# Kernel tuning notes

Hardware: AMD Instinct MI355X
Metric: run time of the kernel (lower is better)

Reference implementation:

```python
import jax, jax.numpy as jnp
import numpy as np

N_HEADS = 16
EPS = 1e-6  # WanSelfAttention passes eps=1e-6 to WanRMSNorm
ROPE_MAX = 1024


def _rmsnorm(v, g):
    # WanRMSNorm: normalize in fp32 over the full `dim`, then scale by weight
    v32 = v.astype(jnp.float32)
    n = v32 * jax.lax.rsqrt(jnp.mean(v32 * v32, axis=-1, keepdims=True) + EPS)
    return n * g


def _rope(x, f, h, w, fc, fs):
    # x: [b, s, n, d] with s == f*h*w. Complex rope: (a+bi) * (cos + i sin)
    b, s, n, d = x.shape
    c = d // 2
    c1 = c - 2 * (c // 3)
    c2 = c // 3

    def build(t):  # t: [ROPE_MAX, c] -> [1, s, 1, c]
        tf, th, tw = t[:, :c1], t[:, c1:c1 + c2], t[:, c1 + c2:]
        pf = jnp.broadcast_to(tf[:f, None, None, :], (f, h, w, c1))
        ph = jnp.broadcast_to(th[None, :h, None, :], (f, h, w, c2))
        pw = jnp.broadcast_to(tw[None, None, :w, :], (f, h, w, c2))
        return jnp.concatenate([pf, ph, pw], axis=-1).reshape(1, f * h * w, 1, c)

    cosv, sinv = build(fc), build(fs)
    xr = x.astype(jnp.float32).reshape(b, s, n, c, 2)
    a, bi = xr[..., 0], xr[..., 1]
    out_r = a * cosv - bi * sinv
    out_i = a * sinv + bi * cosv
    return jnp.stack([out_r, out_i], axis=-1).reshape(b, s, n, d)


def setup_inputs() -> dict:
    key = jax.random.key(0)
    ks = jax.random.split(key, 12)
    b, s, dim = 1, 2048, 2048
    n, d = N_HEADS, 2048 // N_HEADS  # d = 128, c = 64
    f, h, w = 2, 32, 32              # f*h*w == s
    c = d // 2
    c1 = c - 2 * (c // 3)
    c2 = c // 3

    # Realistic rope tables per band (cos/sin of pos * inv_freq)
    pos = np.arange(ROPE_MAX, dtype=np.float64)[:, None]
    ang = []
    for cx in (c1, c2, c2):
        inv = 1.0 / (10000.0 ** (np.arange(cx, dtype=np.float64) / cx))
        ang.append(pos * inv[None, :])
    ang = np.concatenate(ang, axis=1)
    freqs_cos = jnp.asarray(np.cos(ang), dtype=jnp.float32)
    freqs_sin = jnp.asarray(np.sin(ang), dtype=jnp.float32)

    scale = 1.0 / np.sqrt(dim)
    inp = {
        "x": jax.random.normal(ks[0], (b, s, dim), dtype=jnp.float32),
        "freqs_cos": freqs_cos,
        "freqs_sin": freqs_sin,
        "Wq": jax.random.normal(ks[1], (dim, dim), dtype=jnp.float32) * scale,
        "bq": jnp.zeros((dim,), dtype=jnp.float32),
        "Wk": jax.random.normal(ks[2], (dim, dim), dtype=jnp.float32) * scale,
        "bk": jnp.zeros((dim,), dtype=jnp.float32),
        "Wv": jax.random.normal(ks[3], (dim, dim), dtype=jnp.float32) * scale,
        "bv": jnp.zeros((dim,), dtype=jnp.float32),
        "Wo": jax.random.normal(ks[4], (dim, dim), dtype=jnp.float32) * scale,
        "bo": jnp.zeros((dim,), dtype=jnp.float32),
        "gq": jnp.ones((dim,), dtype=jnp.float32),
        "gk": jnp.ones((dim,), dtype=jnp.float32),
        "seq_lens": jnp.array([s], dtype=jnp.int32),
        "f": f,
        "h": h,
        "w": w,
    }
    return inp


def reference(x, freqs_cos, freqs_sin, Wq, bq, Wk, bk, Wv, bv, Wo, bo, gq, gk,
              seq_lens, f, h, w):
    b, s, dim = x.shape
    n = N_HEADS
    d = dim // n

    q = _rmsnorm(x @ Wq.T + bq, gq).reshape(b, s, n, d)
    k = _rmsnorm(x @ Wk.T + bk, gk).reshape(b, s, n, d)
    v = (x @ Wv.T + bv).reshape(b, s, n, d)

    q = _rope(q, f, h, w, freqs_cos, freqs_sin)
    k = _rope(k, f, h, w, freqs_cos, freqs_sin)

    scale = np.float32(1.0 / np.sqrt(d))
    scores = jnp.einsum('bqnd,bknd->bnqk', q, k) * scale  # [b,n,s,s]
    key_mask = jnp.arange(s)[None, :] < seq_lens[:, None]  # [b,s] (k_lens)
    scores = jnp.where(key_mask[:, None, None, :], scores, -jnp.inf)
    probs = jax.nn.softmax(scores, axis=-1)
    out = jnp.einsum('bnqk,bknd->bqnd', probs, v).reshape(b, s, dim)
    return out @ Wo.T + bo
```

## Files before the change

### kernel.cpp

```cpp
#include <hip/hip_runtime.h>
#include <cstdint>
#include <cmath>

typedef unsigned int uint;
typedef unsigned short ushort;
typedef __bf16 bf16_t;
typedef bf16_t bf16x8 __attribute__((ext_vector_type(8)));
typedef float f32x4 __attribute__((ext_vector_type(4)));
typedef float f32x16 __attribute__((ext_vector_type(16)));

#define LOG2E 1.44269504088896340736f

__device__ __forceinline__ ushort f2bf(float f) {
  uint x = __float_as_uint(f);
  x += 0x7fffu + ((x >> 16) & 1u);
  return (ushort)(x >> 16);
}
__device__ __forceinline__ uint pack2(float lo, float hi) {
  return (uint)f2bf(lo) | ((uint)f2bf(hi) << 16);
}
__device__ __forceinline__ uint cvt_pk_bf16(float lo, float hi) {
  uint r;
  asm("v_cvt_pk_bf16_f32 %0, %1, %2" : "=v"(r) : "v"(lo), "v"(hi));
  return r;
}

__device__ __forceinline__ void gload_lds16(const void* gsrc, void* ldsdst) {
  typedef const __attribute__((address_space(1))) unsigned int* gp_t;
  typedef __attribute__((address_space(3))) unsigned int* lp_t;
  __builtin_amdgcn_global_load_lds((gp_t)(uintptr_t)gsrc,
                                   (lp_t)(unsigned int)(uintptr_t)ldsdst,
                                   16, 0, 0);
}

__global__ __launch_bounds__(256) void cvt5(const float* __restrict__ x,
                                            const float* __restrict__ wq,
                                            const float* __restrict__ wk,
                                            const float* __restrict__ wv,
                                            const float* __restrict__ wo,
                                            ushort* __restrict__ xb,
                                            ushort* __restrict__ wqkv,
                                            ushort* __restrict__ wob,
                                            int nx8, int nw8) {
  const int y = blockIdx.y;
  const float* src;
  ushort* dst;
  int n8;
  if (y == 0)      { src = x;  dst = xb;  n8 = nx8; }
  else if (y == 4) { src = wo; dst = wob; n8 = nw8; }
  else {
    src = (y == 1) ? wq : (y == 2) ? wk : wv;
    dst = wqkv + (size_t)(y - 1) * nw8 * 8;
    n8 = nw8;
  }
  int i = blockIdx.x * blockDim.x + threadIdx.x;
  if (i >= n8) return;
  const float4* s4 = (const float4*)src;
  float4 a = s4[i * 2], b = s4[i * 2 + 1];
  uint4 o;
  o.x = pack2(a.x, a.y); o.y = pack2(a.z, a.w);
  o.z = pack2(b.x, b.y); o.w = pack2(b.z, b.w);
  ((uint4*)dst)[i] = o;
}

__global__ __launch_bounds__(512) void gemm_qkv_db(const ushort* __restrict__ A,
                                                   const ushort* __restrict__ B,
                                                   const float* __restrict__ bq,
                                                   const float* __restrict__ bk,
                                                   const float* __restrict__ bv,
                                                   float* __restrict__ qpre,
                                                   float* __restrict__ kpre,
                                                   ushort* __restrict__ Vt,
                                                   int K, int S_) {
  __shared__ __align__(16) unsigned char As[16384];
  __shared__ __align__(16) unsigned char Bs[16384];
  const int t = threadIdx.x, l = t & 63, w = t >> 6;
  const int g = l >> 4, c = l & 15;
  const int wr = w >> 1, wc = w & 1;
  const int tm = blockIdx.y * 128, tn = blockIdx.x * 128;

  const int srow = w * 16 + (l >> 2);
  const int schunk = (l & 3) ^ (srow & 3);
  const ushort* Ag = A + (size_t)(tm + srow) * K + schunk * 8;
  const ushort* Bg = B + (size_t)(tn + srow) * K + schunk * 8;

  f32x4 acc[2][4] = {};

  const int NT = K >> 5;
  gload_lds16(Ag, As + w * 1024);
  gload_lds16(Bg, Bs + w * 1024);

  for (int j = 0; j < NT; ++j) {
    const int buf = j & 1, nb = buf ^ 1;
    if (j + 1 < NT) {
      const int kt1 = (j + 1) << 5;
      gload_lds16(Ag + kt1, As + nb * 8192 + w * 1024);
      gload_lds16(Bg + kt1, Bs + nb * 8192 + w * 1024);
      asm volatile("s_waitcnt vmcnt(2)" ::: "memory");
    } else {
      asm volatile("s_waitcnt vmcnt(0)" ::: "memory");
    }
    __builtin_amdgcn_s_barrier();

    const unsigned char* Ab = As + buf * 8192;
    const unsigned char* Bb = Bs + buf * 8192;
    bf16x8 af[2], bfr[4];
#pragma unroll
    for (int m = 0; m < 2; ++m) {
      int row = wr * 32 + m * 16 + c;
      af[m] = *(const bf16x8*)(Ab + row * 64 + ((g ^ (row & 3)) << 4));
    }
#pragma unroll
    for (int n = 0; n < 4; ++n) {
      int row = wc * 64 + n * 16 + c;
      bfr[n] = *(const bf16x8*)(Bb + row * 64 + ((g ^ (row & 3)) << 4));
    }
#pragma unroll
    for (int m = 0; m < 2; ++m)
#pragma unroll
      for (int n = 0; n < 4; ++n)
        acc[m][n] = __builtin_amdgcn_mfma_f32_16x16x32_bf16(af[m], bfr[n], acc[m][n], 0, 0, 0);

    __builtin_amdgcn_s_barrier();
  }

  const int sel = tn >> 11;
  if (sel < 2) {
    float* outp = sel ? kpre : qpre;
    const float* bias = sel ? bk : bq;
#pragma unroll
    for (int n = 0; n < 4; ++n) {
      int col = (tn & 2047) + wc * 64 + n * 16 + c;
      float bvv = bias[col];
#pragma unroll
      for (int m = 0; m < 2; ++m) {
        int row0 = tm + wr * 32 + m * 16 + g * 4;
#pragma unroll
        for (int i = 0; i < 4; ++i)
          outp[(size_t)(row0 + i) * 2048 + col] = acc[m][n][i] + bvv;
      }
    }
  } else {
#pragma unroll
    for (int n = 0; n < 4; ++n) {
      int colv = (tn - 4096) + wc * 64 + n * 16 + c;
      float bvv = bv[colv];
#pragma unroll
      for (int m = 0; m < 2; ++m) {
        int row0 = tm + wr * 32 + m * 16 + g * 4;
        uint2 o;
        o.x = pack2(acc[m][n][0] + bvv, acc[m][n][1] + bvv);
        o.y = pack2(acc[m][n][2] + bvv, acc[m][n][3] + bvv);
        *(uint2*)(Vt + (size_t)colv * S_ + row0) = o;
      }
    }
  }
}

__global__ __launch_bounds__(512) void gemm_wo_db(const ushort* __restrict__ A,
                                                  const ushort* __restrict__ B,
                                                  float* __restrict__ pbuf, int K) {
  __shared__ __align__(16) unsigned char As[16384];
  __shared__ __align__(16) unsigned char Bs[16384];
  const int t = threadIdx.x, l = t & 63, w = t >> 6;
  const int g = l >> 4, c = l & 15;
  const int wr = w >> 1, wc = w & 1;
  const int tm = blockIdx.y * 128, tn = blockIdx.x * 128;
  const int ks = blockIdx.z;
  const int k0 = ks * (K >> 1);

  const int srow = w * 16 + (l >> 2);
  const int schunk = (l & 3) ^ (srow & 3);
  const ushort* Ag = A + (size_t)(tm + srow) * K + k0 + schunk * 8;
  const ushort* Bg = B + (size_t)(tn + srow) * K + k0 + schunk * 8;

  f32x4 acc[2][4] = {};

  const int NT = K >> 6;
  gload_lds16(Ag, As + w * 1024);
  gload_lds16(Bg, Bs + w * 1024);

  for (int j = 0; j < NT; ++j) {
    const int buf = j & 1, nb = buf ^ 1;
    if (j + 1 < NT) {
      const int kt1 = (j + 1) << 5;
      gload_lds16(Ag + kt1, As + nb * 8192 + w * 1024);
      gload_lds16(Bg + kt1, Bs + nb * 8192 + w * 1024);
      asm volatile("s_waitcnt vmcnt(2)" ::: "memory");
    } else {
      asm volatile("s_waitcnt vmcnt(0)" ::: "memory");
    }
    __builtin_amdgcn_s_barrier();

    const unsigned char* Ab = As + buf * 8192;
    const unsigned char* Bb = Bs + buf * 8192;
    bf16x8 af[2], bfr[4];
#pragma unroll
    for (int m = 0; m < 2; ++m) {
      int row = wr * 32 + m * 16 + c;
      af[m] = *(const bf16x8*)(Ab + row * 64 + ((g ^ (row & 3)) << 4));
    }
#pragma unroll
    for (int n = 0; n < 4; ++n) {
      int row = wc * 64 + n * 16 + c;
      bfr[n] = *(const bf16x8*)(Bb + row * 64 + ((g ^ (row & 3)) << 4));
    }
#pragma unroll
    for (int m = 0; m < 2; ++m)
#pragma unroll
      for (int n = 0; n < 4; ++n)
        acc[m][n] = __builtin_amdgcn_mfma_f32_16x16x32_bf16(af[m], bfr[n], acc[m][n], 0, 0, 0);

    __builtin_amdgcn_s_barrier();
  }

  float* out = pbuf + (size_t)ks * 2048 * 2048;
#pragma unroll
  for (int n = 0; n < 4; ++n) {
    int col = tn + wc * 64 + n * 16 + c;
#pragma unroll
    for (int m = 0; m < 2; ++m) {
      int row0 = tm + wr * 32 + m * 16 + g * 4;
#pragma unroll
      for (int i = 0; i < 4; ++i)
        out[(size_t)(row0 + i) * 2048 + col] = acc[m][n][i];
    }
  }
}

__global__ __launch_bounds__(256) void reduce_wo(const float* __restrict__ p,
                                                 const float* __restrict__ bo,
                                                 float* __restrict__ out, int n4) {
  int i = blockIdx.x * blockDim.x + threadIdx.x;
  if (i >= n4) return;
  float4 a = ((const float4*)p)[i];
  float4 b = ((const float4*)p)[i + n4];
  float4 bb = *(const float4*)(bo + ((i * 4) & 2047));
  float4 o;
  o.x = a.x + b.x + bb.x; o.y = a.y + b.y + bb.y;
  o.z = a.z + b.z + bb.z; o.w = a.w + b.w + bb.w;
  ((float4*)out)[i] = o;
}

__global__ __launch_bounds__(256) void fuse_rms_rope(const float* __restrict__ qpre,
                                                     const float* __restrict__ kpre,
                                                     const float* __restrict__ gq,
                                                     const float* __restrict__ gk,
                                                     const float* __restrict__ fc,
                                                     const float* __restrict__ fs,
                                                     const int* __restrict__ pH,
                                                     const int* __restrict__ pW,
                                                     ushort* __restrict__ Qb,
                                                     ushort* __restrict__ Kb,
                                                     int dim, float foldq) {
  const int which = blockIdx.y;
  const float* pre = which ? kpre : qpre;
  const float* gw = which ? gk : gq;
  ushort* outp = which ? Kb : Qb;
  const float fold = which ? 1.0f : foldq;

  const int p = blockIdx.x, t = threadIdx.x;
  const float* row = pre + (size_t)p * dim;
  float v[8];
  {
    float4 a = *(const float4*)(row + t * 8);
    float4 b = *(const float4*)(row + t * 8 + 4);
    v[0] = a.x; v[1] = a.y; v[2] = a.z; v[3] = a.w;
    v[4] = b.x; v[5] = b.y; v[6] = b.z; v[7] = b.w;
  }
  float ss = 0.f;
#pragma unroll
  for (int i = 0; i < 8; ++i) ss += v[i] * v[i];
#pragma unroll
  for (int off = 32; off; off >>= 1) ss += __shfl_xor(ss, off);
  __shared__ float wsum[4];
  if ((t & 63) == 0) wsum[t >> 6] = ss;
  __syncthreads();
  float rstd = rsqrtf((wsum[0] + wsum[1] + wsum[2] + wsum[3]) * (1.0f / dim) + 1e-6f);
  float gv[8];
  {
    float4 a = *(const float4*)(gw + t * 8);
    float4 b = *(const float4*)(gw + t * 8 + 4);
    gv[0] = a.x; gv[1] = a.y; gv[2] = a.z; gv[3] = a.w;
    gv[4] = b.x; gv[5] = b.y; gv[6] = b.z; gv[7] = b.w;
  }
#pragma unroll
  for (int i = 0; i < 8; ++i) v[i] = v[i] * rstd * gv[i];

  const int H = pH[0], W = pW[0];
  const int hw = H * W;
  const int fr = p / hw;
  const int rem = p - fr * hw;
  const int hh = rem / W;
  const int ww = rem - hh * W;
  const int hd = dim / 16;
  const int cd = hd >> 1;
  const int c2 = cd / 3, c1 = cd - 2 * c2;
  const int j0 = ((t * 8) % hd) >> 1;

  uint ob[4];
#pragma unroll
  for (int q = 0; q < 4; ++q) {
    int j = j0 + q;
    int ri = (j < c1) ? fr : ((j < c1 + c2) ? hh : ww);
    float cs = fc[ri * cd + j];
    float sn = fs[ri * cd + j];
    float a = v[2 * q], b = v[2 * q + 1];
    ob[q] = pack2((a * cs - b * sn) * fold, (a * sn + b * cs) * fold);
  }
  uint4 o4; o4.x = ob[0]; o4.y = ob[1]; o4.z = ob[2]; o4.w = ob[3];
  *(uint4*)(outp + (size_t)p * dim + t * 8) = o4;
}

__global__ __launch_bounds__(512, 2) void attn32(const ushort* __restrict__ Qb,
                                                 const ushort* __restrict__ Kb,
                                                 const ushort* __restrict__ Vt,
                                                 ushort* __restrict__ Ob,
                                                 const int* __restrict__ seq_lens,
                                                 int S_, int DIMc) {
  __shared__ __align__(16) unsigned char smem[66560];
  float* mlbuf = (float*)(smem + 65536);
  const int t = threadIdx.x, l = t & 63, w = t >> 6;
  const int qsub = w & 3, ksp = w >> 2;
  const int h = l >> 5, ql = l & 31;

  const int orig = blockIdx.y * gridDim.x + blockIdx.x;
  const int nwg = gridDim.x * gridDim.y;
  const int lin = (orig & 7) * (nwg >> 3) + (orig >> 3);
  const int q0 = (lin % gridDim.x) * 128;
  const int head = lin / gridDim.x;
  const int kvlen = seq_lens[0];

  unsigned char* sk_s = smem + ksp * 16384;
  unsigned char* sv_s = smem + 32768 + ksp * 16384;

  bf16x8 qf[8];
  {
    const ushort* qp = Qb + (size_t)(q0 + qsub * 32 + ql) * DIMc + head * 128 + h * 8;
#pragma unroll
    for (int s = 0; s < 8; ++s) qf[s] = *(const bf16x8*)(qp + s * 16);
  }

  f32x16 ofr[4] = {};
  float m_run = -1e30f, l_run = 0.f;

  const int nt = (kvlen + 63) >> 6;
  const int half = (nt + 1) >> 1;
  const int tbase = ksp ? half : 0;
  const int mycnt = ksp ? (nt - half) : half;

  for (int tt = 0; tt < half; ++tt) {
    __syncthreads();
    if (tt < mycnt) {
      const int kv0 = (tbase + tt) * 64;
#pragma unroll
      for (int it = 0; it < 4; ++it) {
        int kr = qsub * 16 + it * 4 + (l >> 4);
        int kc = (l & 15) ^ (kr & 15);
        gload_lds16(Kb + (size_t)(kv0 + kr) * DIMc + head * 128 + kc * 8,
                    sk_s + qsub * 4096 + it * 1024);
        int vr = qsub * 32 + it * 8 + (l >> 3);
        int vc = (l & 7) ^ (vr & 7);
        gload_lds16(Vt + (size_t)(head * 128 + vr) * S_ + kv0 + vc * 8,
                    sv_s + qsub * 4096 + it * 1024);
      }
    }
    __syncthreads();
    if (tt >= mycnt) continue;
    const int kv0 = (tbase + tt) * 64;

    f32x16 sfr[2] = {};
    __builtin_amdgcn_s_setprio(1);
#pragma unroll
    for (int kb = 0; kb < 2; ++kb) {
      const unsigned char* kbp = sk_s + (kb * 32 + ql) * 256;
      const int rx = (kb * 32 + ql) & 15;
#pragma unroll
      for (int s = 0; s < 8; ++s) {
        bf16x8 kf = *(const bf16x8*)(kbp + (((s * 2 + h) ^ rx) << 4));
        sfr[kb] = __builtin_amdgcn_mfma_f32_32x32x16_bf16(kf, qf[s], sfr[kb], 0, 0, 0);
      }
    }
    __builtin_amdgcn_s_setprio(0);

    if (kv0 + 64 > kvlen) {
#pragma unroll
      for (int kb = 0; kb < 2; ++kb)
#pragma unroll
        for (int r = 0; r < 16; ++r) {
          int key = kv0 + kb * 32 + (r & 3) + 8 * (r >> 2) + 4 * h;
          if (key >= kvlen) sfr[kb][r] = -1e30f;
        }
    }

    float mt = -1e30f;
#pragma unroll
    for (int kb = 0; kb < 2; ++kb)
#pragma unroll
      for (int r = 0; r < 16; ++r) mt = fmaxf(mt, sfr[kb][r]);
    mt = fmaxf(mt, __shfl_xor(mt, 32));

    if (!__all(mt <= m_run + 8.0f)) {
      float m_new = fmaxf(m_run, mt);
      float fac = __builtin_amdgcn_exp2f(m_run - m_new);
      l_run *= fac;
#pragma unroll
      for (int df = 0; df < 4; ++df) ofr[df] *= fac;
      m_run = m_new;
    }

    float ls = 0.f;
    uint u[2][4][2];
#pragma unroll
    for (int kb = 0; kb < 2; ++kb)
#pragma unroll
      for (int G = 0; G < 4; ++G) {
        float p0 = __builtin_amdgcn_exp2f(sfr[kb][G * 4 + 0] - m_run);
        float p1 = __builtin_amdgcn_exp2f(sfr[kb][G * 4 + 1] - m_run);
        float p2 = __builtin_amdgcn_exp2f(sfr[kb][G * 4 + 2] - m_run);
        float p3 = __builtin_amdgcn_exp2f(sfr[kb][G * 4 + 3] - m_run);
        ls += (p0 + p1) + (p2 + p3);
        u[kb][G][0] = cvt_pk_bf16(p0, p1);
        u[kb][G][1] = cvt_pk_bf16(p2, p3);
      }
    ls += __shfl_xor(ls, 32);
    l_run += ls;

#pragma unroll
    for (int ks = 0; ks < 4; ++ks) {
      const int kb = ks >> 1, G0 = (ks & 1) * 2;
      uint own0 = h ? u[kb][G0 + 1][0] : u[kb][G0][0];
      uint own1 = h ? u[kb][G0 + 1][1] : u[kb][G0][1];
      uint snd0 = h ? u[kb][G0][0] : u[kb][G0 + 1][0];
      uint snd1 = h ? u[kb][G0][1] : u[kb][G0 + 1][1];
      uint rcv0 = __shfl_xor(snd0, 32);
      uint rcv1 = __shfl_xor(snd1, 32);
      union { uint4 q; bf16x8 b; } uu;
      uu.q.x = h ? rcv0 : own0;
      uu.q.y = h ? rcv1 : own1;
      uu.q.z = h ? own0 : rcv0;
      uu.q.w = h ? own1 : rcv1;
      __builtin_amdgcn_s_setprio(1);
#pragma unroll
      for (int df = 0; df < 4; ++df) {
        const int row = df * 32 + ql;
        bf16x8 vf = *(const bf16x8*)(sv_s + row * 128 + (((ks * 2 + h) ^ (row & 7)) << 4));
        ofr[df] = __builtin_amdgcn_mfma_f32_32x32x16_bf16(vf, uu.b, ofr[df], 0, 0, 0);
      }
      __builtin_amdgcn_s_setprio(0);
    }
  }

  __syncthreads();
  if (ksp == 1) {
    if (h == 0) { mlbuf[qsub * 64 + ql] = m_run; mlbuf[qsub * 64 + 32 + ql] = l_run; }
    float* ob = (float*)(smem + qsub * 16384);
#pragma unroll
    for (int df = 0; df < 4; ++df)
#pragma unroll
      for (int r = 0; r < 16; ++r) {
        int d = df * 32 + (r & 3) + 8 * (r >> 2) + 4 * h;
        ob[d * 32 + ql] = ofr[df][r];
      }
  }
  __syncthreads();
  if (ksp == 0) {
    float m2 = mlbuf[qsub * 64 + ql], l2 = mlbuf[qsub * 64 + 32 + ql];
    float mstar = fmaxf(m_run, m2);
    float f1 = __builtin_amdgcn_exp2f(m_run - mstar);
    float f2 = (l2 > 0.f) ? __builtin_amdgcn_exp2f(m2 - mstar) : 0.f;
    float lstar = l_run * f1 + l2 * f2;
    float inv = 1.0f / lstar;
    float a1 = f1 * inv, a2 = f2 * inv;
    const float* ob = (const float*)(smem + qsub * 16384);
    ushort* orow = Ob + (size_t)(q0 + qsub * 32 + ql) * DIMc + head * 128;
#pragma unroll
    for (int df = 0; df < 4; ++df)
#pragma unroll
      for (int G = 0; G < 4; ++G) {
        int d0 = df * 32 + 8 * G + 4 * h;
        float v0 = ofr[df][G * 4 + 0] * a1 + ob[(d0 + 0) * 32 + ql] * a2;
        float v1 = ofr[df][G * 4 + 1] * a1 + ob[(d0 + 1) * 32 + ql] * a2;
        float v2 = ofr[df][G * 4 + 2] * a1 + ob[(d0 + 2) * 32 + ql] * a2;
        float v3 = ofr[df][G * 4 + 3] * a1 + ob[(d0 + 3) * 32 + ql] * a2;
        uint2 o; o.x = pack2(v0, v1); o.y = pack2(v2, v3);
        *(uint2*)(orow + d0) = o;
      }
  }
}

extern "C" void kernel_launch(void* const* d_in, const int* in_sizes, int n_in,
                              void* d_out, int out_size, void* d_ws, size_t ws_size,
                              hipStream_t stream) {
  const float* x  = (const float*)d_in[0];
  const float* fc = (const float*)d_in[1];
  const float* fs = (const float*)d_in[2];
  const float* Wq = (const float*)d_in[3];
  const float* bq = (const float*)d_in[4];
  const float* Wk = (const float*)d_in[5];
  const float* bk = (const float*)d_in[6];
  const float* Wv = (const float*)d_in[7];
  const float* bv = (const float*)d_in[8];
  const float* Wo = (const float*)d_in[9];
  const float* bo = (const float*)d_in[10];
  const float* gq = (const float*)d_in[11];
  const float* gk = (const float*)d_in[12];
  const int* seq  = (const int*)d_in[13];
  const int* pH   = (const int*)d_in[15];
  const int* pW   = (const int*)d_in[16];

  const int DIMc = in_sizes[4];
  const int S_   = in_sizes[0] / DIMc;

  char* ws = (char*)d_ws;
  const size_t MB = 1024ull * 1024ull;
  ushort* xb    = (ushort*)(ws + 0 * MB);
  ushort* Wqkvb = (ushort*)(ws + 8 * MB);
  ushort* Wob   = (ushort*)(ws + 32 * MB);
  float*  qpre  = (float*)(ws + 40 * MB);
  float*  kpre  = (float*)(ws + 56 * MB);
  ushort* Qb    = (ushort*)(ws + 72 * MB);
  ushort* Kb    = (ushort*)(ws + 80 * MB);
  ushort* Vt    = (ushort*)(ws + 88 * MB);
  ushort* Ob    = (ushort*)(ws + 40 * MB);
  float*  pbuf  = (float*)(ws + 56 * MB);

  const int nx8 = (S_ * DIMc) / 8;
  const int nw8 = (DIMc * DIMc) / 8;
  const int nmax = (nx8 > nw8 ? nx8 : nw8);
  cvt5<<<dim3((nmax + 255) / 256, 5), 256, 0, stream>>>(x, Wq, Wk, Wv, Wo,
                                                        xb, Wqkvb, Wob, nx8, nw8);

  gemm_qkv_db<<<dim3(3 * DIMc / 128, S_ / 128), 512, 0, stream>>>(
      xb, Wqkvb, bq, bk, bv, qpre, kpre, Vt, DIMc, S_);

  const float foldq = LOG2E / sqrtf((float)(DIMc / 16));
  fuse_rms_rope<<<dim3(S_, 2), 256, 0, stream>>>(qpre, kpre, gq, gk, fc, fs, pH, pW,
                                                 Qb, Kb, DIMc, foldq);

  attn32<<<dim3(S_ / 128, 16), 512, 0, stream>>>(Qb, Kb, Vt, Ob, seq, S_, DIMc);

  gemm_wo_db<<<dim3(16, 16, 2), 512, 0, stream>>>(Ob, Wob, pbuf, DIMc);
  reduce_wo<<<(S_ * DIMc / 4 + 255) / 256, 256, 0, stream>>>(pbuf, bo, (float*)d_out,
                                                             S_ * DIMc / 4);
}
```

Before: 187.4 us.

## Rewrite QKV GEMM with 256x256 tiles and an 8-wave ping-pong LDS pipeline

Replaces the 128x128, K=32 double-buffered QKV projection GEMM with a 256x256 tile kernel. Each block steps K by 64 and interleaves quarter-tile global-to-LDS staging with MFMA phases, using barriers and s_setprio to hide load latency. Larger tiles raise arithmetic intensity and cut redundant global and LDS traffic. In exchange it uses 128KB of LDS, holds 32 accumulators per thread, and launches only 192 blocks, which may leave compute units idle.

```diff
diff --git a/kernel.cpp b/kernel.cpp
--- a/kernel.cpp
+++ b/kernel.cpp
@@ -63,66 +63,109 @@
   ((uint4*)dst)[i] = o;
 }
 
-__global__ __launch_bounds__(512) void gemm_qkv_db(const ushort* __restrict__ A,
-                                                   const ushort* __restrict__ B,
-                                                   const float* __restrict__ bq,
-                                                   const float* __restrict__ bk,
-                                                   const float* __restrict__ bv,
-                                                   float* __restrict__ qpre,
-                                                   float* __restrict__ kpre,
-                                                   ushort* __restrict__ Vt,
-                                                   int K, int S_) {
-  __shared__ __align__(16) unsigned char As[16384];
-  __shared__ __align__(16) unsigned char Bs[16384];
-  const int t = threadIdx.x, l = t & 63, w = t >> 6;
+__global__ __launch_bounds__(512) void gemm_qkv8p(const ushort* __restrict__ A,
+                                                  const ushort* __restrict__ B,
+                                                  const float* __restrict__ bq,
+                                                  const float* __restrict__ bk,
+                                                  const float* __restrict__ bv,
+                                                  float* __restrict__ qpre,
+                                                  float* __restrict__ kpre,
+                                                  ushort* __restrict__ Vt,
+                                                  int K, int S_) {
+  __shared__ __align__(16) unsigned char ldsA[65536];
+  __shared__ __align__(16) unsigned char ldsB[65536];
+  const int t = threadIdx.x, l = t & 63;
+  const int w = t >> 6;
   const int g = l >> 4, c = l & 15;
-  const int wr = w >> 1, wc = w & 1;
-  const int tm = blockIdx.y * 128, tn = blockIdx.x * 128;
-
-  const int srow = w * 16 + (l >> 2);
-  const int schunk = (l & 3) ^ (srow & 3);
+  const int wr = w >> 2, wc = w & 3;
+  const int tm = blockIdx.y * 256, tn = blockIdx.x * 256;
+
+  const int srow = t >> 3;
+  const int schunk = (t & 7) ^ (srow & 7);
   const ushort* Ag = A + (size_t)(tm + srow) * K + schunk * 8;
   const ushort* Bg = B + (size_t)(tn + srow) * K + schunk * 8;
-
-  f32x4 acc[2][4] = {};
-
-  const int NT = K >> 5;
-  gload_lds16(Ag, As + w * 1024);
-  gload_lds16(Bg, Bs + w * 1024);
-
-  for (int j = 0; j < NT; ++j) {
-    const int buf = j & 1, nb = buf ^ 1;
-    if (j + 1 < NT) {
-      const int kt1 = (j + 1) << 5;
-      gload_lds16(Ag + kt1, As + nb * 8192 + w * 1024);
-      gload_lds16(Bg + kt1, Bs + nb * 8192 + w * 1024);
-      asm volatile("s_waitcnt vmcnt(2)" ::: "memory");
-    } else {
-      asm volatile("s_waitcnt vmcnt(0)" ::: "memory");
-    }
-    __builtin_amdgcn_s_barrier();
-
-    const unsigned char* Ab = As + buf * 8192;
-    const unsigned char* Bb = Bs + buf * 8192;
-    bf16x8 af[2], bfr[4];
-#pragma unroll
-    for (int m = 0; m < 2; ++m) {
-      int row = wr * 32 + m * 16 + c;
-      af[m] = *(const bf16x8*)(Ab + row * 64 + ((g ^ (row & 3)) << 4));
-    }
-#pragma unroll
-    for (int n = 0; n < 4; ++n) {
-      int row = wc * 64 + n * 16 + c;
-      bfr[n] = *(const bf16x8*)(Bb + row * 64 + ((g ^ (row & 3)) << 4));
-    }
-#pragma unroll
-    for (int m = 0; m < 2; ++m)
-#pragma unroll
-      for (int n = 0; n < 4; ++n)
-        acc[m][n] = __builtin_amdgcn_mfma_f32_16x16x32_bf16(af[m], bfr[n], acc[m][n], 0, 0, 0);
-
-    __builtin_amdgcn_s_barrier();
-  }
+  const size_t rK64 = (size_t)64 * K;
+
+#define STG_A(kt, h, q) gload_lds16(Ag + (size_t)(2*(h)+(q)) * rK64 + ((kt) << 6),   \
+    ldsA + ((kt)&1) * 32768 + (h) * 16384 + (q) * 8192 + t * 16)
+#define STG_B(kt, h, q) gload_lds16(Bg + (size_t)(2*(h)+(q)) * rK64 + ((kt) << 6),   \
+    ldsB + ((kt)&1) * 32768 + (h) * 16384 + (q) * 8192 + t * 16)
+
+  f32x4 acc[8][4] = {};
+  bf16x8 af[4][2], bfr[4][2];
+  const int cr = c * 128;
+  const int sw0 = ((0 * 4 + g) ^ (c & 7)) << 4;
+  const int sw1 = ((1 * 4 + g) ^ (c & 7)) << 4;
+
+#define RDA(d, QM) do {                                                              \
+    _Pragma("unroll") for (int mm = 0; mm < 4; ++mm) {                               \
+      const unsigned char* p_ = ldsA + (d)*32768 + wr*16384 + (QM)*8192 + mm*2048 + cr; \
+      af[mm][0] = *(const bf16x8*)(p_ + sw0);                                        \
+      af[mm][1] = *(const bf16x8*)(p_ + sw1); }                                      \
+  } while (0)
+#define RDB(d) do {                                                                  \
+    _Pragma("unroll") for (int nn = 0; nn < 4; ++nn) {                               \
+      const unsigned char* p_ = ldsB + (d)*32768 + (wc>>1)*16384 + (wc&1)*8192 + nn*2048 + cr; \
+      bfr[nn][0] = *(const bf16x8*)(p_ + sw0);                                       \
+      bfr[nn][1] = *(const bf16x8*)(p_ + sw1); }                                     \
+  } while (0)
+#define MM(QM, QN) do {                                                              \
+    __builtin_amdgcn_s_setprio(1);                                                   \
+    _Pragma("unroll") for (int mm = 0; mm < 4; ++mm)                                 \
+    _Pragma("unroll") for (int nn = 0; nn < 2; ++nn) {                               \
+      acc[(QM)*4+mm][(QN)*2+nn] = __builtin_amdgcn_mfma_f32_16x16x32_bf16(           \
+          af[mm][0], bfr[(QN)*2+nn][0], acc[(QM)*4+mm][(QN)*2+nn], 0, 0, 0);         \
+      acc[(QM)*4+mm][(QN)*2+nn] = __builtin_amdgcn_mfma_f32_16x16x32_bf16(           \
+          af[mm][1], bfr[(QN)*2+nn][1], acc[(QM)*4+mm][(QN)*2+nn], 0, 0, 0); }       \
+    __builtin_amdgcn_s_setprio(0);                                                   \
+  } while (0)
+#define BAR() __builtin_amdgcn_s_barrier()
+
+  STG_B(0, 0, 0); STG_B(0, 0, 1); STG_B(0, 1, 0); STG_B(0, 1, 1);
+  STG_A(0, 0, 0); STG_A(0, 1, 0); STG_A(0, 0, 1); STG_A(0, 1, 1);
+  STG_B(1, 0, 0); STG_B(1, 0, 1); STG_B(1, 1, 0); STG_B(1, 1, 1);
+  STG_A(1, 0, 0); STG_A(1, 1, 0);
+  asm volatile("s_waitcnt vmcnt(6)" ::: "memory");
+  BAR();
+
+  const int NITER = K >> 7;
+  for (int i = 0; i < NITER; ++i) {
+    const int k1 = 2 * i + 1, k2 = 2 * i + 2, k3 = 2 * i + 3;
+    const bool st = (i + 1 < NITER);
+    RDA(0, 0); RDB(0);
+    STG_A(k1, 0, 1); STG_A(k1, 1, 1);
+    MM(0, 0); BAR();
+    if (st) { STG_B(k2, 0, 0); STG_B(k2, 0, 1); }
+    MM(0, 1); BAR();
+    RDA(0, 1);
+    if (st) { STG_B(k2, 1, 0); STG_B(k2, 1, 1); }
+    MM(1, 0); BAR();
+    if (st) { STG_A(k2, 0, 0); STG_A(k2, 1, 0); }
+    MM(1, 1);
+    if (st) asm volatile("s_waitcnt vmcnt(6)" ::: "memory");
+    else    asm volatile("s_waitcnt vmcnt(0)" ::: "memory");
+    BAR();
+    RDA(1, 0); RDB(1);
+    if (st) { STG_A(k2, 0, 1); STG_A(k2, 1, 1); }
+    MM(0, 0); BAR();
+    if (st) { STG_B(k3, 0, 0); STG_B(k3, 0, 1); }
+    MM(0, 1); BAR();
+    RDA(1, 1);
+    if (st) { STG_B(k3, 1, 0); STG_B(k3, 1, 1); }
+    MM(1, 0); BAR();
+    if (st) { STG_A(k3, 0, 0); STG_A(k3, 1, 0); }
+    MM(1, 1);
+    if (st) asm volatile("s_waitcnt vmcnt(6)" ::: "memory");
+    else    asm volatile("s_waitcnt vmcnt(0)" ::: "memory");
+    BAR();
+  }
+
+#undef STG_A
+#undef STG_B
+#undef RDA
+#undef RDB
+#undef MM
+#undef BAR
 
   const int sel = tn >> 11;
   if (sel < 2) {
@@ -133,8 +176,8 @@
       int col = (tn & 2047) + wc * 64 + n * 16 + c;
       float bvv = bias[col];
 #pragma unroll
-      for (int m = 0; m < 2; ++m) {
-        int row0 = tm + wr * 32 + m * 16 + g * 4;
+      for (int m = 0; m < 8; ++m) {
+        int row0 = tm + wr * 128 + m * 16 + g * 4;
 #pragma unroll
         for (int i = 0; i < 4; ++i)
           outp[(size_t)(row0 + i) * 2048 + col] = acc[m][n][i] + bvv;
@@ -146,8 +189,8 @@
       int colv = (tn - 4096) + wc * 64 + n * 16 + c;
       float bvv = bv[colv];
 #pragma unroll
-      for (int m = 0; m < 2; ++m) {
-        int row0 = tm + wr * 32 + m * 16 + g * 4;
+      for (int m = 0; m < 8; ++m) {
+        int row0 = tm + wr * 128 + m * 16 + g * 4;
         uint2 o;
         o.x = pack2(acc[m][n][0] + bvv, acc[m][n][1] + bvv);
         o.y = pack2(acc[m][n][2] + bvv, acc[m][n][3] + bvv);
@@ -531,7 +574,7 @@
   cvt5<<<dim3((nmax + 255) / 256, 5), 256, 0, stream>>>(x, Wq, Wk, Wv, Wo,
                                                         xb, Wqkvb, Wob, nx8, nw8);
 
-  gemm_qkv_db<<<dim3(3 * DIMc / 128, S_ / 128), 512, 0, stream>>>(
+  gemm_qkv8p<<<dim3(3 * DIMc / 256, S_ / 256), 512, 0, stream>>>(
       xb, Wqkvb, bq, bk, bv, qpre, kpre, Vt, DIMc, S_);
 
   const float foldq = LOG2E / sqrtf((float)(DIMc / 16));
```

New measurement: 176.5 us. -5.8%, faster.
